# Kernel optimization log

Measured on AMD Instinct MI355X. Metric: run time of the kernel, lower is better.

## Reference

```python
import jax, jax.numpy as jnp
import numpy as np

CTX = 336          # context_length
PRED = 30          # prediction_length
NUM_SAMPLES = 100
LAGS = [1, 2, 3, 4, 5, 6, 7]   # get_lag_indices_v4('B')
N_LAGS_CH = 1 + len(LAGS)      # context itself + lagged copies
N_TF = 4                       # time features
HID = 128
IN_DIM = (N_LAGS_CH + 2 + N_TF) * CTX + PRED + 2 + N_TF * PRED  # 4856
B = 1024
T_PAST = 512


def _extract_lags(past_target):
    # [B, 1+len(LAGS), CTX]: context window shifted back by each lag
    Tp = past_target.shape[1]
    chans = [past_target[:, Tp - CTX - l: Tp - l] for l in [0] + LAGS]
    return jnp.stack(chans, axis=1)


def _rolling_std(ctx):
    # torch loop: rstd[:, i] = ctx[:, max(0, i-4):i+1].std(dim=1) for i >= 2
    # vectorized via cumulative sums; unbiased variance (n-1 denom, Bessel)
    Bn, T = ctx.shape
    z = jnp.zeros((Bn, 1), ctx.dtype)
    cs = jnp.concatenate([z, jnp.cumsum(ctx, axis=1)], axis=1)
    cs2 = jnp.concatenate([z, jnp.cumsum(ctx * ctx, axis=1)], axis=1)
    i = jnp.arange(T)
    a = jnp.maximum(0, i - 4)
    n = (i + 1 - a).astype(ctx.dtype)
    s = cs[:, i + 1] - cs[:, a]
    s2 = cs2[:, i + 1] - cs2[:, a]
    var = (s2 - s * s / n) / jnp.maximum(n - 1.0, 1.0)
    valid = i >= 2
    var_safe = jnp.where(valid, var, 1.0)
    return jnp.where(valid, jnp.sqrt(jnp.clip(var_safe, 1e-12, None)), 0.0)


def _build_context(past_target, past_time_feat):
    ctx = past_target[:, -CTX:]
    lags = _extract_lags(past_target)
    diff = jnp.concatenate([jnp.zeros_like(ctx[:, :1]), ctx[:, 1:] - ctx[:, :-1]], axis=1)
    diff = diff / jnp.clip(jnp.mean(jnp.abs(diff), axis=1, keepdims=True), 1e-6, None)
    rstd = _rolling_std(ctx)
    rstd = rstd / jnp.clip(jnp.mean(jnp.abs(rstd), axis=1, keepdims=True), 1e-6, None)
    ptf = jnp.swapaxes(past_time_feat, 1, 2)  # [B, F, T_past]
    tf_ctx = ptf[:, :, -CTX:]
    return jnp.concatenate([lags, diff[:, None], rstd[:, None], tf_ctx], axis=1)  # [B, 14, CTX]


def _robust_norm(ctx):
    loc = jnp.median(ctx, axis=1)
    scale = jnp.clip(jnp.mean(jnp.abs(ctx - loc[:, None]), axis=1), 1e-6, None)
    return (ctx - loc[:, None]) / scale[:, None], loc, scale


def _forward(past_target, past_time_feat, future_time_feat, W1, b1, W2, b2, W3, b3):
    Bn = past_target.shape[0]
    context = past_target[:, -CTX:]
    _, loc, scale = _robust_norm(context)
    ch = _build_context(past_target, past_time_feat)
    ch = ch.at[:, :N_LAGS_CH].set((ch[:, :N_LAGS_CH] - loc[:, None, None]) / scale[:, None, None])
    ft = jnp.swapaxes(future_time_feat, 1, 2)[:, :, :PRED]  # [B, F, PRED]
    static_feat = jnp.concatenate([ch.reshape(Bn, -1), ft.reshape(Bn, -1)], axis=1)
    th = jnp.ones((Bn, 2), past_target.dtype)  # (t, h) = ones
    z = jax.random.normal(jax.random.key(42), (NUM_SAMPLES, Bn, PRED), dtype=past_target.dtype)

    def step(carry, z_s):
        x = jnp.concatenate([z_s, th, static_feat], axis=1)  # [B, IN_DIM]
        h1 = jax.nn.gelu(x @ W1 + b1)
        h2 = jax.nn.gelu(h1 @ W2 + b2)
        u = h2 @ W3 + b3
        pred = (z_s - u) * scale[:, None] + loc[:, None]  # inverse RobustNorm
        return carry, pred

    _, preds = jax.lax.scan(step, None, z)  # [S, B, PRED]
    return jnp.transpose(preds, (1, 0, 2))  # [B, S, PRED]


def setup_inputs() -> dict:
    key = jax.random.key(0)
    ks = jax.random.split(key, 8)
    return {
        "past_target": jax.random.normal(ks[0], (B, T_PAST), jnp.float32),
        "past_observed_values": jnp.ones((B, T_PAST), jnp.float32),
        "past_time_feat": jax.random.normal(ks[1], (B, T_PAST, N_TF), jnp.float32),
        "future_time_feat": jax.random.normal(ks[2], (B, PRED, N_TF), jnp.float32),
        "W1": 0.02 * jax.random.normal(ks[3], (IN_DIM, HID), jnp.float32),
        "b1": jnp.zeros((HID,), jnp.float32),
        "W2": 0.02 * jax.random.normal(ks[4], (HID, HID), jnp.float32),
        "b2": jnp.zeros((HID,), jnp.float32),
        "W3": 0.02 * jax.random.normal(ks[5], (HID, PRED), jnp.float32),
        "b3": jnp.zeros((PRED,), jnp.float32),
    }


def reference(past_target, past_observed_values, past_time_feat, future_time_feat, W1, b1, W2, b2, W3, b3):
    # past_observed_values is accepted but unused, as in the original forward
    return _forward(past_target, past_time_feat, future_time_feat, W1, b1, W2, b2, W3, b3)
```

## Files before the change

### kernel.cpp

```cpp
#include <hip/hip_runtime.h>
#include <math.h>

#define CTXN 336
#define PREDN 30
#define NSAMP 100
#define BATCH 1024
#define TPAST 512
#define HID 128
#define NTF 4
#define SFK 4826
#define SFKP 4832
#define KC 8
#define KCH 608

#define SFB_OFF    0u
#define W1T_OFF    9895936u
#define LS_OFF_B   11132928u
#define ZBF_OFF    11141120u
#define PART_OFF_B 30801920u
#define WPK_OFF_B  39714816u

#define NB_FEAT 1024
#define NB_W1T  151
#define NB_WPK  16
#define NB_ZGEN 3200
#define NB_PREP (NB_FEAT+NB_W1T+NB_WPK+NB_ZGEN)

#define NB_BASE 512

typedef unsigned short ush;
typedef __attribute__((ext_vector_type(8))) short bf16x8;
typedef __attribute__((ext_vector_type(4))) float f32x4;

__device__ inline unsigned rotl32(unsigned x, unsigned d){ return (x<<d)|(x>>(32u-d)); }

__device__ inline float erfinv_f32(float x){
  float t1 = (1.0f - x)*(1.0f + x);
  float w = -0.69314718056f * __builtin_amdgcn_logf(t1);
  float p;
  if (w < 5.0f) {
    w -= 2.5f;
    p = 2.81022636e-08f;
    p = fmaf(p, w, 3.43273939e-07f);
    p = fmaf(p, w, -3.5233877e-06f);
    p = fmaf(p, w, -4.39150654e-06f);
    p = fmaf(p, w, 0.00021858087f);
    p = fmaf(p, w, -0.00125372503f);
    p = fmaf(p, w, -0.00417768164f);
    p = fmaf(p, w, 0.246640727f);
    p = fmaf(p, w, 1.50140941f);
  } else {
    w = __builtin_amdgcn_sqrtf(w) - 3.0f;
    p = -0.000200214257f;
    p = fmaf(p, w, 0.000100950558f);
    p = fmaf(p, w, 0.00134934322f);
    p = fmaf(p, w, -0.00367342844f);
    p = fmaf(p, w, 0.00573950773f);
    p = fmaf(p, w, -0.0076224613f);
    p = fmaf(p, w, 0.00943887047f);
    p = fmaf(p, w, 1.00167406f);
    p = fmaf(p, w, 2.83297682f);
  }
  return p*x;
}

__device__ inline float gelu_tanh(float x){
  float x2 = x*x;
  float q  = fmaf(0.044715f*x2, x, x);
  float e  = __builtin_amdgcn_exp2f(2.302114202f * q);
  float r  = __builtin_amdgcn_rcpf(e + 1.0f);
  return fmaf(-x, r, x);
}

__device__ inline ush f2bf(float f){
  unsigned u = __float_as_uint(f);
  unsigned r = (u + 0x7FFFu + ((u>>16)&1u)) >> 16;
  return (ush)r;
}
__device__ inline ush f2bf_t(float f){
  return (ush)(__float_as_uint(f) >> 16);
}
__device__ inline float bf2f(ush v){
  return __uint_as_float(((unsigned)v) << 16);
}

__device__ inline unsigned ordf(float f){
  unsigned u = __float_as_uint(f);
  return (u & 0x80000000u) ? ~u : (u | 0x80000000u);
}
__device__ inline float unordf(unsigned ou){
  unsigned u = (ou & 0x80000000u) ? (ou & 0x7FFFFFFFu) : ~ou;
  return __uint_as_float(u);
}

__device__ inline float blockReduceSum256(float v, volatile float* red){
  for (int o=32;o>0;o>>=1) v += __shfl_down(v, o, 64);
  int w = threadIdx.x>>6, lane = threadIdx.x&63;
  __syncthreads();
  if (lane==0) red[w]=v;
  __syncthreads();
  return red[0]+red[1]+red[2]+red[3];
}

__device__ inline unsigned blockReduceMin256(unsigned v, volatile unsigned* redu){
  for (int o=32;o>0;o>>=1){ unsigned t = __shfl_down(v, o, 64); v = (t<v)?t:v; }
  int w = threadIdx.x>>6, lane = threadIdx.x&63;
  __syncthreads();
  if (lane==0) redu[w]=v;
  __syncthreads();
  unsigned a = redu[0], b = redu[1], c = redu[2], d = redu[3];
  unsigned ab = (a<b)?a:b, cd = (c<d)?c:d;
  return (ab<cd)?ab:cd;
}

__device__ inline void tf_rounds4(unsigned (&x0)[4], unsigned (&x1)[4],
                                  int r0, int r1, int r2, int r3){
  #pragma unroll
  for (int i=0;i<4;i++){ x0[i]+=x1[i]; x1[i]=rotl32(x1[i],r0); x1[i]^=x0[i]; }
  #pragma unroll
  for (int i=0;i<4;i++){ x0[i]+=x1[i]; x1[i]=rotl32(x1[i],r1); x1[i]^=x0[i]; }
  #pragma unroll
  for (int i=0;i<4;i++){ x0[i]+=x1[i]; x1[i]=rotl32(x1[i],r2); x1[i]^=x0[i]; }
  #pragma unroll
  for (int i=0;i<4;i++){ x0[i]+=x1[i]; x1[i]=rotl32(x1[i],r3); x1[i]^=x0[i]; }
}

__global__ __launch_bounds__(256) void prep_kernel(
    const float* __restrict__ pt, const float* __restrict__ ptf,
    const float* __restrict__ ftf, const float* __restrict__ W1,
    const float* __restrict__ W2, const float* __restrict__ W3,
    char* __restrict__ wsb)
{
  __shared__ float seg[343];
  __shared__ __attribute__((aligned(16))) float segA[CTXN];
  __shared__ float dbuf[CTXN];
  __shared__ float rbuf[CTXN];
  __shared__ float red[4];
  __shared__ unsigned redu[4];
  __shared__ int bins[16];
  const int bid = blockIdx.x;
  const int tid = threadIdx.x;

  if (bid >= NB_FEAT){
    const int b2id = bid - NB_FEAT;
    if (b2id < NB_W1T){
      ush* w1t = (ush*)(wsb + W1T_OFF);
      const int k0 = b2id*32;
      const int col = tid >> 1;
      const int kh  = (tid & 1)*16;
      ush v[16];
      #pragma unroll
      for (int j=0;j<16;j++){
        int k = k0 + kh + j;
        v[j] = (k < SFK) ? f2bf(W1[(size_t)(30+k)*HID + col]) : (ush)0;
      }
      ush* dst = w1t + (size_t)col*SFKP + k0 + kh;
      *(uint4*)dst       = *(const uint4*)&v[0];
      *(uint4*)(dst + 8) = *(const uint4*)&v[8];
      return;
    }
    if (b2id < NB_W1T + NB_WPK){
      ush* wb = (ush*)(wsb + WPK_OFF_B);
      int t2 = (b2id - NB_W1T)*256 + tid;
      { int col = t2>>5, k = t2&31;
        wb[t2] = (k<30) ? f2bf(W1[(size_t)k*HID + col]) : (ush)0; }
      #pragma unroll
      for (int j=0;j<4;j++){
        int i = j*4096 + t2;
        int col = i>>7, k = i&127;
        wb[4096 + i] = f2bf(W2[(size_t)k*HID + col]);
      }
      { int col = t2>>7, k = t2&127;
        wb[20480 + t2] = (col<30) ? f2bf(W3[(size_t)k*PREDN + col]) : (ush)0; }
      return;
    }
    {
      ush* zb = (ush*)(wsb + ZBF_OFF);
      const int g  = (b2id - NB_W1T - NB_WPK)*256 + tid;
      const int sb = g >> 3;
      const int t0 = (g & 7) * 4;
      const int s = sb >> 10, b = sb & 1023;
      const unsigned jb = (unsigned)(s*30720 + b*30 + t0);

      const unsigned k0=0u, k1=42u, k2 = k0^k1^0x1BD11BDAu;
      unsigned x0[4], x1[4];
      #pragma unroll
      for (int i=0;i<4;i++){ x0[i] = k0; x1[i] = (jb + (unsigned)i) + k1; }

      tf_rounds4(x0,x1,13,15,26,6);
      #pragma unroll
      for (int i=0;i<4;i++){ x0[i]+=k1; x1[i]+=k2+1u; }
      tf_rounds4(x0,x1,17,29,16,24);
      #pragma unroll
      for (int i=0;i<4;i++){ x0[i]+=k2; x1[i]+=k0+2u; }
      tf_rounds4(x0,x1,13,15,26,6);
      #pragma unroll
      for (int i=0;i<4;i++){ x0[i]+=k0; x1[i]+=k1+3u; }
      tf_rounds4(x0,x1,17,29,16,24);
      #pragma unroll
      for (int i=0;i<4;i++){ x0[i]+=k1; x1[i]+=k2+4u; }
      tf_rounds4(x0,x1,13,15,26,6);
      #pragma unroll
      for (int i=0;i<4;i++){ x0[i]+=k2; x1[i]+=k0+5u; }

      const float LO = -0.99999994f;
      float vout[4];
      #pragma unroll
      for (int i=0;i<4;i++){
        unsigned bits = x0[i]^x1[i];
        float f = __uint_as_float((bits>>9)|0x3f800000u) - 1.0f;
        float u = fmaxf(LO, f*2.0f + LO);
        vout[i] = (t0 + i < 30) ? 1.41421356f * erfinv_f32(u) : 0.f;
      }
      uint2 pv;
      pv.x = (unsigned)f2bf(vout[0]) | ((unsigned)f2bf(vout[1]) << 16);
      pv.y = (unsigned)f2bf(vout[2]) | ((unsigned)f2bf(vout[3]) << 16);
      *(uint2*)(zb + (size_t)sb*32 + t0) = pv;
      return;
    }
  }

  const int b = bid;
  for (int i = tid; i < 343; i += 256) seg[i] = pt[(size_t)b*TPAST + 169 + i];
  __syncthreads();
  for (int i = tid; i < CTXN; i += 256) segA[i] = seg[7+i];
  __syncthreads();

  const unsigned oe0 = ordf(segA[tid]);
  const bool has1 = (tid < CTXN - 256);
  const unsigned oe1 = has1 ? ordf(segA[256 + tid]) : 0u;

  unsigned pfx = 0u; int kk = 167;
  #pragma unroll
  for (int shift = 28; shift >= 0; shift -= 4){
    __syncthreads();
    if (tid < 16) bins[tid] = 0;
    __syncthreads();
    const unsigned hi_mask = (shift==28) ? 0u : (0xFFFFFFFFu << (shift+4));
    if (((oe0 ^ pfx) & hi_mask) == 0) atomicAdd(&bins[(oe0>>shift)&15], 1);
    if (has1 && (((oe1 ^ pfx) & hi_mask) == 0)) atomicAdd(&bins[(oe1>>shift)&15], 1);
    __syncthreads();
    int cum = 0, sel = 15;
    #pragma unroll
    for (int bb = 0; bb < 16; bb++){
      int c = bins[bb];
      if (kk < cum + c){ sel = bb; break; }
      cum += c;
    }
    kk -= cum;
    pfx |= ((unsigned)sel) << shift;
  }
  const float v167 = unordf(pfx);

  float cle = ((oe0 <= pfx) ? 1.f : 0.f) + ((has1 && oe1 <= pfx) ? 1.f : 0.f);
  cle = blockReduceSum256(cle, red);
  unsigned mg = (oe0 > pfx) ? oe0 : 0xFFFFFFFFu;
  if (has1 && oe1 > pfx && oe1 < mg) mg = oe1;
  mg = blockReduceMin256(mg, redu);
  const float v168 = (cle >= 168.5f) ? v167 : unordf(mg);
  const float loc = 0.5f*(v167 + v168);

  float part = 0.f;
  for (int t=tid;t<CTXN;t+=256) part += fabsf(segA[t]-loc);
  part = blockReduceSum256(part, red);
  float scale = fmaxf(part/(float)CTXN, 1e-6f);

  float pd = 0.f;
  for (int t=tid;t<CTXN;t+=256){
    float d = (t==0)?0.f:(seg[7+t]-seg[6+t]);
    dbuf[t]=d; pd += fabsf(d);
  }
  pd = blockReduceSum256(pd, red);
  float dden = fmaxf(pd/(float)CTXN, 1e-6f);

  float pr = 0.f;
  for (int t=tid;t<CTXN;t+=256){
    int a = t-4; if (a<0) a=0;
    int n = t+1-a;
    float s=0.f, s2s=0.f;
    for (int jj=a;jj<=t;jj++){ float v=seg[7+jj]; s+=v; s2s+=v*v; }
    float fn = (float)n;
    float var = (s2s - s*s/fn) / fmaxf(fn-1.f, 1.f);
    float r = (t>=2)? sqrtf(fmaxf(var,1e-12f)) : 0.f;
    rbuf[t]=r; pr += r;
  }
  pr = blockReduceSum256(pr, red);
  float rden = fmaxf(pr/(float)CTXN, 1e-6f);
  __syncthreads();

  ush* sf = (ush*)(wsb + SFB_OFF) + (size_t)b*SFKP;
  float* ls = (float*)(wsb + LS_OFF_B);
  if (tid<2) sf[tid] = (ush)0x3F80;
  if (tid<SFKP-SFK) sf[SFK+tid] = 0;
  float iscale = 1.0f/scale, iden = 1.0f/dden, irden = 1.0f/rden;
  for (int t=tid;t<CTXN;t+=256){
    #pragma unroll
    for (int c=0;c<8;c++)
      sf[2 + c*CTXN + t] = f2bf((seg[7 - c + t] - loc)*iscale);
    sf[2+8*CTXN+t] = f2bf(dbuf[t]*iden);
    sf[2+9*CTXN+t] = f2bf(rbuf[t]*irden);
    float4 tf4 = *(const float4*)(ptf + (size_t)b*TPAST*NTF + (size_t)(176+t)*NTF);
    sf[2 + 10*CTXN + t] = f2bf(tf4.x);
    sf[2 + 11*CTXN + t] = f2bf(tf4.y);
    sf[2 + 12*CTXN + t] = f2bf(tf4.z);
    sf[2 + 13*CTXN + t] = f2bf(tf4.w);
  }
  for (int i=tid;i<NTF*PREDN;i+=256){
    int f = i/PREDN, t = i - f*PREDN;
    sf[2+14*CTXN + i] = f2bf(ftf[(size_t)b*PREDN*NTF + t*NTF + f]);
  }
  if (tid==0){ ls[b] = loc; ls[BATCH + b] = scale; }
}

__global__ __launch_bounds__(256) void base_kernel(
    const char* __restrict__ wsb, float* __restrict__ partb)
{
  const ush* sfb = (const ush*)(wsb + SFB_OFF);
  const ush* w1t = (const ush*)(wsb + W1T_OFF);
  const int tid = threadIdx.x;
  const int w = tid>>6, l = tid&63;
  const int li = l&15, lk = l>>4;
  const int rb = (blockIdx.x & 63)*16;
  const int kc = blockIdx.x >> 6;
  const int kbeg = kc*KCH;
  const int kend = min(SFKP, kbeg+KCH);

  f32x4 acc0 = {0.f,0.f,0.f,0.f}, acc1 = {0.f,0.f,0.f,0.f};
  const ush* ap  = sfb + (size_t)(rb + li)*SFKP + lk*8;
  const ush* b0p = w1t + (size_t)(w*32 + li)*SFKP + lk*8;
  const ush* b1p = b0p + (size_t)16*SFKP;

  #pragma unroll 4
  for (int kk0 = kbeg; kk0 < kend; kk0 += 32){
    bf16x8 a  = *(const bf16x8*)(ap  + kk0);
    bf16x8 b0 = *(const bf16x8*)(b0p + kk0);
    bf16x8 b1 = *(const bf16x8*)(b1p + kk0);
    acc0 = __builtin_amdgcn_mfma_f32_16x16x32_bf16(a, b0, acc0, 0, 0, 0);
    acc1 = __builtin_amdgcn_mfma_f32_16x16x32_bf16(a, b1, acc1, 0, 0, 0);
  }
  float* p = partb + ((size_t)kc*BATCH + rb)*HID;
  #pragma unroll
  for (int q=0;q<4;q++){
    p[(lk*4+q)*HID + w*32      + li] = acc0[q];
    p[(lk*4+q)*HID + w*32 + 16 + li] = acc1[q];
  }
}

__global__ __launch_bounds__(256) void mlp_kernel(
    const char* __restrict__ wsb, const float* __restrict__ b1v,
    const float* __restrict__ b2v, const float* __restrict__ b3v,
    float* __restrict__ out)
{
  const int tid = threadIdx.x;
  const int wv = tid>>6, l = tid&63;
  const int li = l&15, lk = l>>4;
  const int r0 = blockIdx.x*16;
  const int sg = blockIdx.y;

  const float* ls    = (const float*)(wsb + LS_OFF_B);
  const ush*   zbf   = (const ush*)(wsb + ZBF_OFF);
  const float* partb = (const float*)(wsb + PART_OFF_B);
  const char*  wpkc  = wsb + WPK_OFF_B;

  __shared__ __attribute__((aligned(16))) ush  wlds[24576];
  __shared__ __attribute__((aligned(16))) float blds[2048];
  __shared__ __attribute__((aligned(16))) ush  hb4[4][2048];
  char* hb = (char*)hb4[wv];
  char* wl = (char*)wlds;

  #pragma unroll
  for (int i=0;i<12;i++){
    int byte = (i*256 + tid)*16;
    int swz;
    if (byte < 8192){ int col = byte>>6; swz = byte ^ ((col&3)<<4); }
    else if (byte < 40960){ int X = byte - 8192; int col = X>>8; swz = 8192 + (X ^ ((col&7)<<4)); }
    else { int X = byte - 40960; int col = X>>8; swz = 40960 + (X ^ ((col&7)<<4)); }
    *(float4*)(wl + swz) = *(const float4*)(wpkc + byte);
  }
  #pragma unroll
  for (int k=0;k<8;k++){
    int i = k*256 + tid;
    float acc = b1v[i & 127];
    #pragma unroll
    for (int kc=0;kc<KC;kc++)
      acc += partb[(size_t)kc*BATCH*HID + (size_t)r0*HID + i];
    blds[i] = acc;
  }
  __syncthreads();

  float b2r[8];
  #pragma unroll
  for (int ct=0; ct<8; ct++) b2r[ct] = b2v[ct*16 + li];
  float b3r[2];
  #pragma unroll
  for (int ct3=0; ct3<2; ct3++){
    int col = ct3*16 + li;
    b3r[ct3] = (col < PREDN) ? b3v[col] : 0.f;
  }
  float loc4[4], scl4[4];
  #pragma unroll
  for (int q=0;q<4;q++){
    int gb = r0 + lk*4 + q;
    loc4[q] = ls[gb];
    scl4[q] = ls[BATCH + gb];
  }
  const int swzli  = (li&7)<<4;
  const int swzli3 = (li&3)<<4;

  #pragma unroll
  for (int u=0; u<4; u++){
    const int s = sg + 8*(wv + 4*u);
    if (s >= NSAMP) continue;

    bf16x8 az = *(const bf16x8*)&zbf[((size_t)(s*BATCH + r0 + li))*32 + lk*8];
    float zep[2][4];
    #pragma unroll
    for (int q=0;q<4;q++){
      const ush* zr2 = zbf + ((size_t)(s*BATCH + r0 + lk*4 + q))*32;
      zep[0][q] = bf2f(zr2[li]);
      zep[1][q] = bf2f(zr2[16 + li]);
    }

    f32x4 acc[8];
    #pragma unroll
    for (int ct=0; ct<8; ct++){
      #pragma unroll
      for (int q=0;q<4;q++)
        acc[ct][q] = blds[(lk*4+q)*HID + ct*16 + li];
    }

    #pragma unroll
    for (int ct=0; ct<8; ct++){
      bf16x8 w1f = *(const bf16x8*)(wl + (((ct*16+li)*64 + lk*16) ^ swzli3));
      acc[ct] = __builtin_amdgcn_mfma_f32_16x16x32_bf16(az, w1f, acc[ct], 0, 0, 0);
    }
    #pragma unroll
    for (int ct=0; ct<8; ct++){
      int col2 = (ct*16 + li)*2;
      #pragma unroll
      for (int q=0;q<4;q++){
        int r = lk*4 + q;
        *(ush*)(hb + r*256 + (col2 ^ ((r&7)<<4))) = f2bf_t(gelu_tanh(acc[ct][q]));
      }
    }

    f32x4 acc2[8];
    #pragma unroll
    for (int ct=0; ct<8; ct++){
      acc2[ct][0]=b2r[ct]; acc2[ct][1]=b2r[ct]; acc2[ct][2]=b2r[ct]; acc2[ct][3]=b2r[ct];
    }
    #pragma unroll
    for (int ks=0; ks<4; ks++){
      bf16x8 a2 = *(const bf16x8*)(hb + li*256 + ((ks*64 + lk*16) ^ swzli));
      #pragma unroll
      for (int ct=0; ct<8; ct++){
        bf16x8 w2f = *(const bf16x8*)(wl + 8192 + (((ct*16+li)*256 + ks*64 + lk*16) ^ swzli));
        acc2[ct] = __builtin_amdgcn_mfma_f32_16x16x32_bf16(a2, w2f, acc2[ct], 0, 0, 0);
      }
    }
    #pragma unroll
    for (int ct=0; ct<8; ct++){
      int col2 = (ct*16 + li)*2;
      #pragma unroll
      for (int q=0;q<4;q++){
        int r = lk*4 + q;
        *(ush*)(hb + r*256 + (col2 ^ ((r&7)<<4))) = f2bf_t(gelu_tanh(acc2[ct][q]));
      }
    }

    f32x4 acc3[2];
    #pragma unroll
    for (int ct3=0; ct3<2; ct3++){
      acc3[ct3][0]=b3r[ct3]; acc3[ct3][1]=b3r[ct3];
      acc3[ct3][2]=b3r[ct3]; acc3[ct3][3]=b3r[ct3];
    }
    #pragma unroll
    for (int ks=0; ks<4; ks++){
      bf16x8 a3 = *(const bf16x8*)(hb + li*256 + ((ks*64 + lk*16) ^ swzli));
      #pragma unroll
      for (int ct3=0; ct3<2; ct3++){
        bf16x8 w3f = *(const bf16x8*)(wl + 40960 + (((ct3*16+li)*256 + ks*64 + lk*16) ^ swzli));
        acc3[ct3] = __builtin_amdgcn_mfma_f32_16x16x32_bf16(a3, w3f, acc3[ct3], 0, 0, 0);
      }
    }

    #pragma unroll
    for (int ct3=0; ct3<2; ct3++){
      int col3 = ct3*16 + li;
      if (col3 < PREDN){
        #pragma unroll
        for (int q=0;q<4;q++){
          int gb = r0 + lk*4 + q;
          out[(size_t)gb*(NSAMP*PREDN) + s*PREDN + col3] =
              (zep[ct3][q] - acc3[ct3][q])*scl4[q] + loc4[q];
        }
      }
    }
  }
}

extern "C" void kernel_launch(void* const* d_in, const int* in_sizes, int n_in,
                              void* d_out, int out_size, void* d_ws, size_t ws_size,
                              hipStream_t stream) {
  (void)in_sizes; (void)n_in; (void)out_size; (void)ws_size;
  const float* pt  = (const float*)d_in[0];
  const float* ptf = (const float*)d_in[2];
  const float* ftf = (const float*)d_in[3];
  const float* W1  = (const float*)d_in[4];
  const float* b1  = (const float*)d_in[5];
  const float* W2  = (const float*)d_in[6];
  const float* b2  = (const float*)d_in[7];
  const float* W3  = (const float*)d_in[8];
  const float* b3  = (const float*)d_in[9];
  float* out = (float*)d_out;
  char* wsb  = (char*)d_ws;

  hipLaunchKernelGGL(prep_kernel, dim3(NB_PREP), dim3(256), 0, stream,
                     pt, ptf, ftf, W1, W2, W3, wsb);
  hipLaunchKernelGGL(base_kernel, dim3(NB_BASE), dim3(256), 0, stream,
                     wsb, (float*)(wsb + PART_OFF_B));
  hipLaunchKernelGGL(mlp_kernel, dim3(64, 8), dim3(256), 0, stream,
                     wsb, b1, b2, b3, out);
}
```

Before: 51.73 us.

## Shrink mlp LDS footprint, read W1/W3 from global, make erfinv wave-uniform

The mlp kernel now stages only W2 in LDS and reads the small W1 and W3 fragments straight from global memory. The layer-1 bias/partial buffer is stored as bf16 instead of fp32, and the b2, b3 and loc/scale values are reloaded inside the sample loop rather than held in registers. Together these cut LDS use and register pressure, aiming for higher occupancy, at the cost of extra global loads per sample and bf16 rounding of the layer-1 partial sums. In prep, erfinv always evaluates the central polynomial and runs the tail branch only if some lane needs it, and a redundant segA copy with its barrier is removed.

Result: slower. 53.86 us (+4.1%).

```diff
diff --git a/kernel.cpp b/kernel.cpp
--- a/kernel.cpp
+++ b/kernel.cpp
@@ -37,29 +37,28 @@
 __device__ inline float erfinv_f32(float x){
   float t1 = (1.0f - x)*(1.0f + x);
   float w = -0.69314718056f * __builtin_amdgcn_logf(t1);
-  float p;
-  if (w < 5.0f) {
-    w -= 2.5f;
-    p = 2.81022636e-08f;
-    p = fmaf(p, w, 3.43273939e-07f);
-    p = fmaf(p, w, -3.5233877e-06f);
-    p = fmaf(p, w, -4.39150654e-06f);
-    p = fmaf(p, w, 0.00021858087f);
-    p = fmaf(p, w, -0.00125372503f);
-    p = fmaf(p, w, -0.00417768164f);
-    p = fmaf(p, w, 0.246640727f);
-    p = fmaf(p, w, 1.50140941f);
-  } else {
-    w = __builtin_amdgcn_sqrtf(w) - 3.0f;
-    p = -0.000200214257f;
-    p = fmaf(p, w, 0.000100950558f);
-    p = fmaf(p, w, 0.00134934322f);
-    p = fmaf(p, w, -0.00367342844f);
-    p = fmaf(p, w, 0.00573950773f);
-    p = fmaf(p, w, -0.0076224613f);
-    p = fmaf(p, w, 0.00943887047f);
-    p = fmaf(p, w, 1.00167406f);
-    p = fmaf(p, w, 2.83297682f);
+  float wc = w - 2.5f;
+  float p = 2.81022636e-08f;
+  p = fmaf(p, wc, 3.43273939e-07f);
+  p = fmaf(p, wc, -3.5233877e-06f);
+  p = fmaf(p, wc, -4.39150654e-06f);
+  p = fmaf(p, wc, 0.00021858087f);
+  p = fmaf(p, wc, -0.00125372503f);
+  p = fmaf(p, wc, -0.00417768164f);
+  p = fmaf(p, wc, 0.246640727f);
+  p = fmaf(p, wc, 1.50140941f);
+  if (__any(w >= 5.0f)) {
+    float ws = __builtin_amdgcn_sqrtf(w) - 3.0f;
+    float p2 = -0.000200214257f;
+    p2 = fmaf(p2, ws, 0.000100950558f);
+    p2 = fmaf(p2, ws, 0.00134934322f);
+    p2 = fmaf(p2, ws, -0.00367342844f);
+    p2 = fmaf(p2, ws, 0.00573950773f);
+    p2 = fmaf(p2, ws, -0.0076224613f);
+    p2 = fmaf(p2, ws, 0.00943887047f);
+    p2 = fmaf(p2, ws, 1.00167406f);
+    p2 = fmaf(p2, ws, 2.83297682f);
+    p = (w < 5.0f) ? p : p2;
   }
   return p*x;
 }
@@ -132,7 +131,6 @@
     char* __restrict__ wsb)
 {
   __shared__ float seg[343];
-  __shared__ __attribute__((aligned(16))) float segA[CTXN];
   __shared__ float dbuf[CTXN];
   __shared__ float rbuf[CTXN];
   __shared__ float red[4];
@@ -223,12 +221,10 @@
   const int b = bid;
   for (int i = tid; i < 343; i += 256) seg[i] = pt[(size_t)b*TPAST + 169 + i];
   __syncthreads();
-  for (int i = tid; i < CTXN; i += 256) segA[i] = seg[7+i];
-  __syncthreads();
-
-  const unsigned oe0 = ordf(segA[tid]);
+
+  const unsigned oe0 = ordf(seg[7+tid]);
   const bool has1 = (tid < CTXN - 256);
-  const unsigned oe1 = has1 ? ordf(segA[256 + tid]) : 0u;
+  const unsigned oe1 = has1 ? ordf(seg[7+256+tid]) : 0u;
 
   unsigned pfx = 0u; int kk = 167;
   #pragma unroll
@@ -261,7 +257,7 @@
   const float loc = 0.5f*(v167 + v168);
 
   float part = 0.f;
-  for (int t=tid;t<CTXN;t+=256) part += fabsf(segA[t]-loc);
+  for (int t=tid;t<CTXN;t+=256) part += fabsf(seg[7+t]-loc);
   part = blockReduceSum256(part, red);
   float scale = fmaxf(part/(float)CTXN, 1e-6f);
 
@@ -361,21 +357,20 @@
   const ush*   zbf   = (const ush*)(wsb + ZBF_OFF);
   const float* partb = (const float*)(wsb + PART_OFF_B);
   const char*  wpkc  = wsb + WPK_OFF_B;
-
-  __shared__ __attribute__((aligned(16))) ush  wlds[24576];
-  __shared__ __attribute__((aligned(16))) float blds[2048];
+  const ush*   wpk   = (const ush*)wpkc;
+
+  __shared__ __attribute__((aligned(16))) ush  wlds[16384];
+  __shared__ __attribute__((aligned(16))) ush  blds[2048];
   __shared__ __attribute__((aligned(16))) ush  hb4[4][2048];
   char* hb = (char*)hb4[wv];
   char* wl = (char*)wlds;
 
   #pragma unroll
-  for (int i=0;i<12;i++){
+  for (int i=0;i<8;i++){
     int byte = (i*256 + tid)*16;
-    int swz;
-    if (byte < 8192){ int col = byte>>6; swz = byte ^ ((col&3)<<4); }
-    else if (byte < 40960){ int X = byte - 8192; int col = X>>8; swz = 8192 + (X ^ ((col&7)<<4)); }
-    else { int X = byte - 40960; int col = X>>8; swz = 40960 + (X ^ ((col&7)<<4)); }
-    *(float4*)(wl + swz) = *(const float4*)(wpkc + byte);
+    int col = byte>>8;
+    int swz = byte ^ ((col&7)<<4);
+    *(float4*)(wl + swz) = *(const float4*)(wpkc + 8192 + byte);
   }
   #pragma unroll
   for (int k=0;k<8;k++){
@@ -384,28 +379,11 @@
     #pragma unroll
     for (int kc=0;kc<KC;kc++)
       acc += partb[(size_t)kc*BATCH*HID + (size_t)r0*HID + i];
-    blds[i] = acc;
-  }
-  __syncthreads();
-
-  float b2r[8];
-  #pragma unroll
-  for (int ct=0; ct<8; ct++) b2r[ct] = b2v[ct*16 + li];
-  float b3r[2];
-  #pragma unroll
-  for (int ct3=0; ct3<2; ct3++){
-    int col = ct3*16 + li;
-    b3r[ct3] = (col < PREDN) ? b3v[col] : 0.f;
-  }
-  float loc4[4], scl4[4];
-  #pragma unroll
-  for (int q=0;q<4;q++){
-    int gb = r0 + lk*4 + q;
-    loc4[q] = ls[gb];
-    scl4[q] = ls[BATCH + gb];
-  }
-  const int swzli  = (li&7)<<4;
-  const int swzli3 = (li&3)<<4;
+    blds[i] = f2bf(acc);
+  }
+  __syncthreads();
+
+  const int swzli = (li&7)<<4;
 
   #pragma unroll
   for (int u=0; u<4; u++){
@@ -426,12 +404,12 @@
     for (int ct=0; ct<8; ct++){
       #pragma unroll
       for (int q=0;q<4;q++)
-        acc[ct][q] = blds[(lk*4+q)*HID + ct*16 + li];
+        acc[ct][q] = bf2f(blds[(lk*4+q)*HID + ct*16 + li]);
     }
 
     #pragma unroll
     for (int ct=0; ct<8; ct++){
-      bf16x8 w1f = *(const bf16x8*)(wl + (((ct*16+li)*64 + lk*16) ^ swzli3));
+      bf16x8 w1f = *(const bf16x8*)&wpk[(ct*16+li)*32 + lk*8];
       acc[ct] = __builtin_amdgcn_mfma_f32_16x16x32_bf16(az, w1f, acc[ct], 0, 0, 0);
     }
     #pragma unroll
@@ -447,14 +425,15 @@
     f32x4 acc2[8];
     #pragma unroll
     for (int ct=0; ct<8; ct++){
-      acc2[ct][0]=b2r[ct]; acc2[ct][1]=b2r[ct]; acc2[ct][2]=b2r[ct]; acc2[ct][3]=b2r[ct];
+      float bb = b2v[ct*16 + li];
+      acc2[ct][0]=bb; acc2[ct][1]=bb; acc2[ct][2]=bb; acc2[ct][3]=bb;
     }
     #pragma unroll
     for (int ks=0; ks<4; ks++){
       bf16x8 a2 = *(const bf16x8*)(hb + li*256 + ((ks*64 + lk*16) ^ swzli));
       #pragma unroll
       for (int ct=0; ct<8; ct++){
-        bf16x8 w2f = *(const bf16x8*)(wl + 8192 + (((ct*16+li)*256 + ks*64 + lk*16) ^ swzli));
+        bf16x8 w2f = *(const bf16x8*)(wl + (((ct*16+li)*256 + ks*64 + lk*16) ^ swzli));
         acc2[ct] = __builtin_amdgcn_mfma_f32_16x16x32_bf16(a2, w2f, acc2[ct], 0, 0, 0);
       }
     }
@@ -471,15 +450,16 @@
     f32x4 acc3[2];
     #pragma unroll
     for (int ct3=0; ct3<2; ct3++){
-      acc3[ct3][0]=b3r[ct3]; acc3[ct3][1]=b3r[ct3];
-      acc3[ct3][2]=b3r[ct3]; acc3[ct3][3]=b3r[ct3];
+      int col = ct3*16 + li;
+      float bb = (col < PREDN) ? b3v[col] : 0.f;
+      acc3[ct3][0]=bb; acc3[ct3][1]=bb; acc3[ct3][2]=bb; acc3[ct3][3]=bb;
     }
     #pragma unroll
     for (int ks=0; ks<4; ks++){
       bf16x8 a3 = *(const bf16x8*)(hb + li*256 + ((ks*64 + lk*16) ^ swzli));
       #pragma unroll
       for (int ct3=0; ct3<2; ct3++){
-        bf16x8 w3f = *(const bf16x8*)(wl + 40960 + (((ct3*16+li)*256 + ks*64 + lk*16) ^ swzli));
+        bf16x8 w3f = *(const bf16x8*)&wpk[20480 + (ct3*16+li)*128 + ks*32 + lk*8];
         acc3[ct3] = __builtin_amdgcn_mfma_f32_16x16x32_bf16(a3, w3f, acc3[ct3], 0, 0, 0);
       }
     }
@@ -492,7 +472,7 @@
         for (int q=0;q<4;q++){
           int gb = r0 + lk*4 + q;
           out[(size_t)gb*(NSAMP*PREDN) + s*PREDN + col3] =
-              (zep[ct3][q] - acc3[ct3][q])*scl4[q] + loc4[q];
+              (zep[ct3][q] - acc3[ct3][q])*ls[BATCH + gb] + ls[gb];
         }
       }
     }
```
